# Performance work log

Measured on AMD Instinct MI355X. Metric: run time of the kernel, lower is better.

The kernel has to match this reference:

```python
import jax, jax.numpy as jnp
import numpy as np

T_Q, N_M, D = 2000, 100000, 1024

def setup_inputs() -> dict:
    key = jax.random.key(0)
    k1, k2, k3 = jax.random.split(key, 3)
    return {
        "query_seq": jax.random.normal(k1, (T_Q, D), dtype=jnp.float32),
        "matching_set": jax.random.normal(k2, (N_M, D), dtype=jnp.float32),
        "synth_set": jax.random.normal(k3, (N_M, D), dtype=jnp.float32),
        "topk": 4,
    }

def reference(query_seq, matching_set, synth_set, topk):
    # kNN-VC match: cosine distance, top-k nearest, mean of synth vectors.
    eps = jnp.asarray(1e-12, query_seq.dtype)
    q = query_seq / jnp.maximum(jnp.linalg.norm(query_seq, axis=-1, keepdims=True), eps)
    m = matching_set / jnp.maximum(jnp.linalg.norm(matching_set, axis=-1, keepdims=True), eps)
    dists = 1.0 - jnp.einsum("qd,nd->qn", q, m)  # (T_q, N_m) cosine distance
    _, idx = jax.lax.top_k(-dists, topk)          # k smallest distances
    # gather-average over selected synth vectors -> (T_q, D)
    out = jnp.mean(synth_set[idx], axis=1)
    return out
```

## Files before the change

kernel.cpp:

```cpp
#include <hip/hip_runtime.h>
#include <math.h>

#define T_Q    2000
#define N_M    100000
#define D_DIM  1024
#define QTILES 16
#define NTILES 782
#define MPAD   (NTILES * 128)
#define BK     32
#define KSTEPS (D_DIM / BK)
#define KST3   32
#define LDH    40
#define SSW    72
#define NC     16
#define QPAD   2048
#define TK     4

typedef _Float16 f16x8 __attribute__((ext_vector_type(8)));
typedef _Float16 f16x4 __attribute__((ext_vector_type(4)));
typedef float    f32x4 __attribute__((ext_vector_type(4)));
typedef unsigned int u32;

struct __align__(8) Cand { float v; int i; };
static_assert(sizeof(Cand) == 8, "cand size");

__device__ __forceinline__ bool better(float av, int ai, float bv, int bi) {
    return (av > bv) || (av == bv && ai < bi);
}

__device__ __forceinline__ f32x4 zero4() {
    f32x4 z; z[0] = 0.f; z[1] = 0.f; z[2] = 0.f; z[3] = 0.f; return z;
}

__device__ __forceinline__ void gload16(const _Float16* g, _Float16* l) {
    const __attribute__((address_space(1))) u32* gp =
        (const __attribute__((address_space(1))) u32*)g;
    __attribute__((address_space(3))) u32* lp =
        (__attribute__((address_space(3))) u32*)l;
    __builtin_amdgcn_global_load_lds(gp, lp, 16, 0, 0);
}

__device__ __forceinline__ int swz_s(int row) {
    return (row & 3) ^ ((row >> 2) & 1);
}

__global__ __launch_bounds__(256)
void knn_qcvt(const float* __restrict__ Qm, _Float16* __restrict__ Qh)
{
    const size_t base = (size_t)blockIdx.x * 2048 + (size_t)threadIdx.x * 8;
    const int row = (int)(base >> 10);
    const int hr  = (int)(base & 1023);
    f16x8 h;
    if (row < T_Q) {
        f32x4 a = *(const f32x4*)(Qm + base);
        f32x4 b = *(const f32x4*)(Qm + base + 4);
#pragma unroll
        for (int j = 0; j < 4; ++j) { h[j] = (_Float16)a[j]; h[4 + j] = (_Float16)b[j]; }
    } else {
#pragma unroll
        for (int j = 0; j < 8; ++j) h[j] = (_Float16)0.f;
    }
    const int g = hr >> 3;
    const int p = (g & ~3) | ((g & 3) ^ swz_s(row));
    *(f16x8*)(Qh + ((size_t)row << 10) + p * 8) = h;
}

__global__ __launch_bounds__(256)
void knn_qcvt_plain(const float* __restrict__ Qm, _Float16* __restrict__ Qh)
{
    const size_t base = (size_t)blockIdx.x * 2048 + (size_t)threadIdx.x * 8;
    const int row = (int)(base >> 10);
    f16x8 h;
    if (row < T_Q) {
        f32x4 a = *(const f32x4*)(Qm + base);
        f32x4 b = *(const f32x4*)(Qm + base + 4);
#pragma unroll
        for (int j = 0; j < 4; ++j) { h[j] = (_Float16)a[j]; h[4 + j] = (_Float16)b[j]; }
    } else {
#pragma unroll
        for (int j = 0; j < 8; ++j) h[j] = (_Float16)0.f;
    }
    *(f16x8*)(Qh + base) = h;
}

__global__ __launch_bounds__(256)
void knn_mcvt(const float* __restrict__ Mm, _Float16* __restrict__ Mh)
{
    const int wid  = threadIdx.x >> 6;
    const int lane = threadIdx.x & 63;
    const int r    = blockIdx.x * 4 + wid;
    f16x8 h0, h1;
    if (r < N_M) {
        const f32x4* mp = (const f32x4*)(Mm + (size_t)r * D_DIM) + lane * 4;
        f32x4 v0 = mp[0], v1 = mp[1], v2 = mp[2], v3 = mp[3];
        float ss = 0.f;
#pragma unroll
        for (int u = 0; u < 4; ++u)
            ss += v0[u] * v0[u] + v1[u] * v1[u] + v2[u] * v2[u] + v3[u] * v3[u];
#pragma unroll
        for (int off = 1; off <= 32; off <<= 1) ss += __shfl_xor(ss, off, 64);
        const float inv = ss > 0.f ? rsqrtf(ss) : 0.f;
#pragma unroll
        for (int u = 0; u < 4; ++u) {
            h0[u]     = (_Float16)(v0[u] * inv);
            h0[4 + u] = (_Float16)(v1[u] * inv);
            h1[u]     = (_Float16)(v2[u] * inv);
            h1[4 + u] = (_Float16)(v3[u] * inv);
        }
    } else {
#pragma unroll
        for (int j = 0; j < 8; ++j) { h0[j] = (_Float16)0.f; h1[j] = (_Float16)0.f; }
    }
    const int s  = swz_s(r);
    const int g0 = 2 * lane;
    const int g1 = g0 + 1;
    const int p0 = (g0 & ~3) | ((g0 & 3) ^ s);
    const int p1 = (g1 & ~3) | ((g1 & 3) ^ s);
    _Float16* base = Mh + (size_t)r * D_DIM;
    *(f16x8*)(base + p0 * 8) = h0;
    *(f16x8*)(base + p1 * 8) = h1;
}

__global__ __launch_bounds__(256, 4)
void knn_gemm_select_h(const _Float16* __restrict__ Qh,
                       const _Float16* __restrict__ Mh,
                       Cand* __restrict__ cand, int tpbn, int nsuper)
{
    __shared__ _Float16 As[2][128][32];
    __shared__ _Float16 Bs[2][128][32];

    const int bid   = blockIdx.x;
    const int c8    = bid & 7;
    const int jj0   = bid >> 3;
    const int qtile = jj0 & 15;
    const int sup   = c8 + 8 * (jj0 >> 4);

    const int nt0 = sup * tpbn;
    int nt1 = nt0 + tpbn;
    if (nt1 > NTILES) nt1 = NTILES;

    const int tid  = threadIdx.x;
    const int lane = tid & 63;
    const int wid  = tid >> 6;
    const int wr   = wid >> 1;
    const int wc   = wid & 1;
    const int l15  = lane & 15;
    const int lg   = lane >> 4;

    const int owner = wr * 4 + lg;

    float rv[4][TK]; int ri[4][TK];
#pragma unroll
    for (int q = 0; q < 4; ++q)
#pragma unroll
        for (int k = 0; k < TK; ++k) { rv[q][k] = -INFINITY; ri[q][k] = 0; }

    if (nt0 >= nt1) {
#pragma unroll
        for (int q = 0; q < 4; ++q) {
            const int qg = qtile * 128 + wc * 64 + q * 16 + l15;
            Cand* dst = cand + (((size_t)qg * nsuper + sup) * 8 + owner) * TK;
#pragma unroll
            for (int k = 0; k < TK; ++k) { Cand c; c.v = rv[q][k]; c.i = ri[q][k]; dst[k] = c; }
        }
        return;
    }

    const int srow   = tid >> 2;
    const int schunk = tid & 3;

    const _Float16* Bb = Qh + ((size_t)(qtile * 128 + srow) << 10) + schunk * 8;

    const int cp = (lg ^ (l15 & 3) ^ ((l15 >> 2) & 1)) * 8;

#define ISSUE_STEP(Abase, koff, bi) do {                                   \
        _Float16* ad_ = &As[bi][0][0] + tid * 8;                           \
        _Float16* bd_ = &Bs[bi][0][0] + tid * 8;                           \
        gload16((Abase) + (koff),               ad_);                      \
        gload16((Abase) + (64 << 10) + (koff),  ad_ + 2048);               \
        gload16(Bb + (koff),                    bd_);                      \
        gload16(Bb + (64 << 10) + (koff),       bd_ + 2048);               \
    } while (0)

    const _Float16* Ab = Mh + ((size_t)(nt0 * 128 + srow) << 10) + schunk * 8;
    int buf = 0;

    ISSUE_STEP(Ab, 0, 0);
    __syncthreads();

#pragma unroll 1
    for (int ntile = nt0; ntile < nt1; ++ntile) {
        const _Float16* AbNext = Ab + ((size_t)128 << 10);

        f32x4 acc[4][4];
#pragma unroll
        for (int i = 0; i < 4; ++i)
#pragma unroll
            for (int j = 0; j < 4; ++j) acc[i][j] = zero4();

#pragma unroll 1
        for (int t = 0; t < KST3; ++t) {
            if (t + 1 < KST3)            ISSUE_STEP(Ab, (t + 1) * 32, buf ^ 1);
            else if (ntile + 1 < nt1)    ISSUE_STEP(AbNext, 0, buf ^ 1);

            f16x8 af[4], bf[4];
#pragma unroll
            for (int f = 0; f < 4; ++f) {
                af[f] = *(const f16x8*)&As[buf][wr * 64 + f * 16 + l15][cp];
                bf[f] = *(const f16x8*)&Bs[buf][wc * 64 + f * 16 + l15][cp];
            }
#pragma unroll
            for (int i = 0; i < 4; ++i)
#pragma unroll
                for (int j = 0; j < 4; ++j)
                    acc[i][j] = __builtin_amdgcn_mfma_f32_16x16x32_f16(
                        af[i], bf[j], acc[i][j], 0, 0, 0);

            __syncthreads();
            buf ^= 1;
        }
        Ab = AbNext;

        const int rowbase = ntile * 128 + wr * 64 + lg * 4;
#pragma unroll
        for (int q = 0; q < 4; ++q) {
            float mx = acc[0][q][0];
#pragma unroll
            for (int i = 0; i < 4; ++i)
#pragma unroll
                for (int r = 0; r < 4; ++r) mx = fmaxf(mx, acc[i][q][r]);
            if (mx >= rv[q][TK - 1]) {
#pragma unroll
                for (int i = 0; i < 4; ++i)
#pragma unroll
                    for (int r = 0; r < 4; ++r) {
                        const int ng = rowbase + i * 16 + r;
                        float cv = acc[i][q][r];
                        if (ng < N_M && better(cv, ng, rv[q][TK - 1], ri[q][TK - 1])) {
                            int ci = ng;
#pragma unroll
                            for (int k = 0; k < TK; ++k) {
                                bool b = better(cv, ci, rv[q][k], ri[q][k]);
                                float nv = b ? cv : rv[q][k]; int ni = b ? ci : ri[q][k];
                                float ov = b ? rv[q][k] : cv; int oi = b ? ri[q][k] : ci;
                                rv[q][k] = nv; ri[q][k] = ni; cv = ov; ci = oi;
                            }
                        }
                    }
            }
        }
    }
#undef ISSUE_STEP

#pragma unroll
    for (int q = 0; q < 4; ++q) {
        const int qg = qtile * 128 + wc * 64 + q * 16 + l15;
        Cand* dst = cand + (((size_t)qg * nsuper + sup) * 8 + owner) * TK;
#pragma unroll
        for (int k = 0; k < TK; ++k) {
            Cand c; c.v = rv[q][k]; c.i = ri[q][k];
            dst[k] = c;
        }
    }
}

__global__ __launch_bounds__(64)
void knn_top16(const Cand* __restrict__ cand, int* __restrict__ top_idx, int ncand)
{
    __shared__ float lv[64][NC];
    __shared__ int   li[64][NC];

    const int q = blockIdx.x;
    const int lane = threadIdx.x;
    const Cand* rowp = cand + (size_t)q * ncand;

    float tv[NC]; int ti[NC];
#pragma unroll
    for (int k = 0; k < NC; ++k) { tv[k] = -INFINITY; ti[k] = 0; }

#pragma unroll 1
    for (int e = lane; e < ncand; e += 64) {
        Cand c = rowp[e];
        if (better(c.v, c.i, tv[NC - 1], ti[NC - 1])) {
            float cv = c.v; int ci = c.i;
#pragma unroll
            for (int k = 0; k < NC; ++k) {
                bool b = better(cv, ci, tv[k], ti[k]);
                float nv = b ? cv : tv[k]; int ni = b ? ci : ti[k];
                float ov = b ? tv[k] : cv; int oi = b ? ti[k] : ci;
                tv[k] = nv; ti[k] = ni; cv = ov; ci = oi;
            }
        }
    }

#pragma unroll
    for (int k = 0; k < NC; ++k) { lv[lane][k] = tv[k]; li[lane][k] = ti[k]; }
    __syncthreads();

    if (lane == 0) {
#pragma unroll 1
        for (int l = 1; l < 64; ++l) {
#pragma unroll 1
            for (int k = 0; k < NC; ++k) {
                float v = lv[l][k]; int i = li[l][k];
                if (!better(v, i, tv[NC - 1], ti[NC - 1])) break;
                float cv = v; int ci = i;
#pragma unroll
                for (int kk = 0; kk < NC; ++kk) {
                    bool b = better(cv, ci, tv[kk], ti[kk]);
                    float nv = b ? cv : tv[kk]; int ni = b ? ci : ti[kk];
                    float ov = b ? tv[kk] : cv; int oi = b ? ti[kk] : ci;
                    tv[kk] = nv; ti[kk] = ni; cv = ov; ci = oi;
                }
            }
        }
#pragma unroll
        for (int k = 0; k < NC; ++k) top_idx[q * NC + k] = ti[k];
    }
}

__global__ __launch_bounds__(256)
void knn_rescore(const float* __restrict__ Qm, const float* __restrict__ Mm,
                 const float* __restrict__ Sm, const int* __restrict__ topk_p,
                 const int* __restrict__ top_idx, float* __restrict__ outp)
{
    const int q   = blockIdx.x;
    const int tid = threadIdx.x;
    const int wid = tid >> 6, lane = tid & 63;

    __shared__ double sval[NC];
    __shared__ int    sidx[NC];
    __shared__ int    chosen[NC];

    int k = *topk_p;
    if (k > NC) k = NC;
    if (k < 1)  k = 1;

    const float* qrow = Qm + (size_t)q * D_DIM;
#pragma unroll 1
    for (int ci = wid; ci < NC; ci += 4) {
        int idx = top_idx[q * NC + ci];
        if (idx < 0)    idx = 0;
        if (idx >= N_M) idx = N_M - 1;
        const f32x4* mp = (const f32x4*)(Mm + (size_t)idx * D_DIM) + lane * 4;
        const f32x4* qp = (const f32x4*)qrow + lane * 4;
        double dot = 0.0, ss = 0.0;
#pragma unroll
        for (int j = 0; j < 4; ++j) {
            f32x4 mv = mp[j], qv = qp[j];
#pragma unroll
            for (int u = 0; u < 4; ++u) {
                dot += (double)mv[u] * (double)qv[u];
                ss  += (double)mv[u] * (double)mv[u];
            }
        }
#pragma unroll
        for (int off = 1; off <= 32; off <<= 1) {
            dot += __shfl_xor(dot, off, 64);
            ss  += __shfl_xor(ss, off, 64);
        }
        if (lane == 0) { sval[ci] = ss > 0.0 ? dot / sqrt(ss) : -1e300; sidx[ci] = idx; }
    }
    __syncthreads();

    if (tid == 0) {
        unsigned used = 0;
        for (int j = 0; j < k; ++j) {
            int best = -1;
            for (int i = 0; i < NC; ++i) {
                if (used & (1u << i)) continue;
                if (best < 0 || sval[i] > sval[best] ||
                    (sval[i] == sval[best] && sidx[i] < sidx[best])) best = i;
            }
            used |= 1u << best;
            chosen[j] = sidx[best];
        }
    }
    __syncthreads();

    const int d0 = tid * 4;
    f32x4 a = zero4();
    for (int j = 0; j < k; ++j) {
        f32x4 s4 = *(const f32x4*)(Sm + (size_t)chosen[j] * D_DIM + d0);
        a = a + s4;
    }
    const float inv = 1.0f / (float)k;
    a = a * inv;
    *(f32x4*)(outp + (size_t)q * D_DIM + d0) = a;
}

__global__ __launch_bounds__(256)
void knn_norms(const float* __restrict__ Mm, float* __restrict__ invn)
{
    const int wid  = threadIdx.x >> 6;
    const int lane = threadIdx.x & 63;
    const int r    = blockIdx.x * 4 + wid;
    if (r >= N_M) return;
    const f32x4* mp = (const f32x4*)(Mm + (size_t)r * D_DIM) + lane * 4;
    float ss = 0.f;
#pragma unroll
    for (int j = 0; j < 4; ++j) {
        f32x4 v = mp[j];
#pragma unroll
        for (int u = 0; u < 4; ++u) ss += v[u] * v[u];
    }
#pragma unroll
    for (int off = 1; off <= 32; off <<= 1) ss += __shfl_xor(ss, off, 64);
    if (lane == 0) invn[r] = ss > 0.f ? rsqrtf(ss) : 0.f;
}

__global__ __launch_bounds__(256)
void knn_gemm_select(const _Float16* __restrict__ Qh, const float* __restrict__ Mm,
                     const float* __restrict__ invn, Cand* __restrict__ cand,
                     int tpbn, int nsuper)
{
    __shared__ _Float16 As[128][LDH];
    __shared__ _Float16 Bs[128][LDH];
    __shared__ _Float16 Ss[128][SSW];
    __shared__ float    sinv[128];

    const int qtile = blockIdx.x & (QTILES - 1);
    const int sup   = blockIdx.x >> 4;
    const int nt0   = sup * tpbn;
    int nt1 = nt0 + tpbn;
    if (nt1 > NTILES) nt1 = NTILES;

    const int tid = threadIdx.x;
    const int row = tid >> 1;
    const int kh  = tid & 1;

    const int qrow_g = qtile * 128 + row;
    const _Float16* bbase = Qh + (size_t)qrow_g * D_DIM + kh * 16;

    const int lane = tid & 63;
    const int wid  = tid >> 6;
    const int wr   = wid >> 1;
    const int wc   = wid & 1;
    const int l15  = lane & 15;
    const int lg   = lane >> 4;

    float rv[NC]; int ri[NC];
#pragma unroll
    for (int k = 0; k < NC; ++k) { rv[k] = -INFINITY; ri[k] = 0; }

#pragma unroll 1
    for (int ntile = nt0; ntile < nt1; ++ntile) {
        const int nrow_g = ntile * 128 + row;
        const bool a_ok  = nrow_g < N_M;
        const float* abase = Mm + (size_t)nrow_g * D_DIM + kh * 16;

        f32x4 acc[4][4];
#pragma unroll
        for (int i = 0; i < 4; ++i)
#pragma unroll
            for (int j = 0; j < 4; ++j) acc[i][j] = zero4();

        f32x4 ar[4];
        f16x8 brh[2];
#pragma unroll
        for (int i = 0; i < 4; ++i) ar[i] = a_ok ? ((const f32x4*)abase)[i] : zero4();
        brh[0] = *(const f16x8*)(bbase);
        brh[1] = *(const f16x8*)(bbase + 8);

#pragma unroll 1
        for (int t = 0; t < KSTEPS; ++t) {
            __syncthreads();

            f16x8 ha0, ha1;
#pragma unroll
            for (int i = 0; i < 2; ++i)
#pragma unroll
                for (int j = 0; j < 4; ++j) {
                    ha0[i * 4 + j] = (_Float16)ar[i][j];
                    ha1[i * 4 + j] = (_Float16)ar[i + 2][j];
                }
            *(f16x8*)&As[row][kh * 16]     = ha0;
            *(f16x8*)&As[row][kh * 16 + 8] = ha1;
            *(f16x8*)&Bs[row][kh * 16]     = brh[0];
            *(f16x8*)&Bs[row][kh * 16 + 8] = brh[1];

            __syncthreads();

            if (t + 1 < KSTEPS) {
                const float*    ap = abase + (t + 1) * BK;
                const _Float16* bp = bbase + (t + 1) * BK;
#pragma unroll
                for (int i = 0; i < 4; ++i) ar[i] = a_ok ? ((const f32x4*)ap)[i] : zero4();
                brh[0] = *(const f16x8*)(bp);
                brh[1] = *(const f16x8*)(bp + 8);
            }

            f16x8 af[4], bf[4];
#pragma unroll
            for (int f = 0; f < 4; ++f) {
                af[f] = *(const f16x8*)&As[wr * 64 + f * 16 + l15][lg * 8];
                bf[f] = *(const f16x8*)&Bs[wc * 64 + f * 16 + l15][lg * 8];
            }
#pragma unroll
            for (int i = 0; i < 4; ++i)
#pragma unroll
                for (int j = 0; j < 4; ++j)
                    acc[i][j] = __builtin_amdgcn_mfma_f32_16x16x32_f16(
                        af[i], bf[j], acc[i][j], 0, 0, 0);
        }

        if (tid < 128) {
            const int r = ntile * 128 + tid;
            sinv[tid] = (r < N_M) ? invn[r] : 0.f;
        }

#pragma unroll 1
        for (int h = 0; h < 2; ++h) {
            __syncthreads();
            if (wr == h) {
#pragma unroll
                for (int fr = 0; fr < 4; ++fr)
#pragma unroll
                    for (int fc = 0; fc < 4; ++fc) {
                        f16x4 v;
#pragma unroll
                        for (int r = 0; r < 4; ++r) v[r] = (_Float16)acc[fr][fc][r];
                        *(f16x4*)&Ss[wc * 64 + fc * 16 + l15][fr * 16 + lg * 4] = v;
                    }
            }
            __syncthreads();

            if (tid < 128) {
                const int base = ntile * 128 + h * 64;
                int nval = N_M - base;
                if (nval > 64) nval = 64;
#pragma unroll 1
                for (int c = 0; c < nval; c += 8) {
                    f16x8 sv = *(const f16x8*)&Ss[tid][c];
                    f32x4 sa = *(const f32x4*)&sinv[h * 64 + c];
                    f32x4 sb = *(const f32x4*)&sinv[h * 64 + c + 4];
                    const int lim = (nval - c >= 8) ? 8 : (nval - c);
                    float s[8];
#pragma unroll
                    for (int j = 0; j < 4; ++j) {
                        s[j]     = (float)sv[j] * sa[j];
                        s[4 + j] = (float)sv[4 + j] * sb[j];
                    }
                    if (lim < 8)
#pragma unroll
                        for (int j = 0; j < 8; ++j)
                            if (j >= lim) s[j] = -INFINITY;
                    float m01 = fmaxf(s[0], s[1]), m23 = fmaxf(s[2], s[3]);
                    float m45 = fmaxf(s[4], s[5]), m67 = fmaxf(s[6], s[7]);
                    float mx = fmaxf(fmaxf(m01, m23), fmaxf(m45, m67));
                    if (mx >= rv[NC - 1]) {
#pragma unroll 1
                        for (int j = 0; j < 8; ++j) {
                            if (j >= lim) break;
                            float cv = s[j]; int ci = base + c + j;
                            if (better(cv, ci, rv[NC - 1], ri[NC - 1])) {
#pragma unroll
                                for (int k = 0; k < NC; ++k) {
                                    bool b = better(cv, ci, rv[k], ri[k]);
                                    float nv = b ? cv : rv[k]; int ni = b ? ci : ri[k];
                                    float ov = b ? rv[k] : cv; int oi = b ? ri[k] : ci;
                                    rv[k] = nv; ri[k] = ni; cv = ov; ci = oi;
                                }
                            }
                        }
                    }
                }
            }
        }
    }

    if (tid < 128) {
        const int qg = qtile * 128 + tid;
        Cand* dst = cand + ((size_t)qg * nsuper + sup) * NC;
#pragma unroll
        for (int k = 0; k < NC; ++k) { Cand c; c.v = rv[k]; c.i = ri[k]; dst[k] = c; }
    }
}

#define FNC 8
__global__ __launch_bounds__(256)
void knn_all(const float* __restrict__ Qm, const float* __restrict__ Mm,
             const float* __restrict__ Sm, const int* __restrict__ topk_p,
             float* __restrict__ outp)
{
    __shared__ float  qs[D_DIM];
    __shared__ float  wv[4][FNC];
    __shared__ int    wi[4][FNC];
    __shared__ int    cand8[FNC];
    __shared__ double dval[FNC];
    __shared__ int    chosen[FNC];
    __shared__ int    sk;

    const int q    = blockIdx.x;
    const int tid  = threadIdx.x;
    const int wid  = tid >> 6;
    const int lane = tid & 63;

    for (int i = tid; i < D_DIM / 4; i += 256)
        ((f32x4*)qs)[i] = ((const f32x4*)(Qm + (size_t)q * D_DIM))[i];
    __syncthreads();

    float tv[FNC]; int ti[FNC];
#pragma unroll
    for (int k = 0; k < FNC; ++k) { tv[k] = -INFINITY; ti[k] = 0; }

    for (int r = wid; r < N_M; r += 4) {
        const f32x4* mp = (const f32x4*)(Mm + (size_t)r * D_DIM) + lane * 4;
        const f32x4* qp = (const f32x4*)qs + lane * 4;
        float dot = 0.f, ss = 0.f;
#pragma unroll
        for (int j = 0; j < 4; ++j) {
            f32x4 mv = mp[j], qv = qp[j];
#pragma unroll
            for (int u = 0; u < 4; ++u) { dot += mv[u] * qv[u]; ss += mv[u] * mv[u]; }
        }
#pragma unroll
        for (int off = 1; off <= 32; off <<= 1) {
            dot += __shfl_xor(dot, off, 64);
            ss  += __shfl_xor(ss,  off, 64);
        }
        float s = ss > 0.f ? dot * rsqrtf(ss) : -INFINITY;
        if (better(s, r, tv[FNC - 1], ti[FNC - 1])) {
            float cv = s; int ci = r;
#pragma unroll
            for (int k = 0; k < FNC; ++k) {
                bool b = better(cv, ci, tv[k], ti[k]);
                float nv = b ? cv : tv[k]; int ni = b ? ci : ti[k];
                float ov = b ? tv[k] : cv; int oi = b ? ti[k] : ci;
                tv[k] = nv; ti[k] = ni; cv = ov; ci = oi;
            }
        }
    }

    if (lane == 0)
#pragma unroll
        for (int k = 0; k < FNC; ++k) { wv[wid][k] = tv[k]; wi[wid][k] = ti[k]; }
    __syncthreads();

    if (tid == 0) {
        unsigned used = 0;
        for (int j = 0; j < FNC; ++j) {
            float bv = -INFINITY; int bi = 0; int bs = -1;
            for (int s = 0; s < 4 * FNC; ++s) {
                if (used & (1u << s)) continue;
                float v = wv[s >> 3][s & 7]; int i = wi[s >> 3][s & 7];
                if (bs < 0 || better(v, i, bv, bi)) { bv = v; bi = i; bs = s; }
            }
            used |= 1u << bs;
            cand8[j] = bi;
        }
        int kk = *topk_p;
        if (kk < 1) kk = 1;
        if (kk > FNC) kk = FNC;
        sk = kk;
    }
    __syncthreads();

    for (int ci = wid; ci < FNC; ci += 4) {
        int idx = cand8[ci];
        if (idx < 0)     idx = 0;
        if (idx >= N_M)  idx = N_M - 1;
        const f32x4* mp = (const f32x4*)(Mm + (size_t)idx * D_DIM) + lane * 4;
        const f32x4* qp = (const f32x4*)qs + lane * 4;
        double dot = 0.0, ss = 0.0;
#pragma unroll
        for (int j = 0; j < 4; ++j) {
            f32x4 mv = mp[j], qv = qp[j];
#pragma unroll
            for (int u = 0; u < 4; ++u) {
                dot += (double)mv[u] * (double)qv[u];
                ss  += (double)mv[u] * (double)mv[u];
            }
        }
#pragma unroll
        for (int off = 1; off <= 32; off <<= 1) {
            dot += __shfl_xor(dot, off, 64);
            ss  += __shfl_xor(ss, off, 64);
        }
        if (lane == 0) dval[ci] = ss > 0.0 ? dot / sqrt(ss) : -1e300;
    }
    __syncthreads();

    if (tid == 0) {
        int kk = sk;
        unsigned used = 0;
        for (int j = 0; j < kk; ++j) {
            int best = -1;
            for (int i = 0; i < FNC; ++i) {
                if (used & (1u << i)) continue;
                if (best < 0 || dval[i] > dval[best] ||
                    (dval[i] == dval[best] && cand8[i] < cand8[best])) best = i;
            }
            used |= 1u << best;
            chosen[j] = cand8[best];
        }
    }
    __syncthreads();

    const int kk = sk;
    const int d0 = tid * 4;
    f32x4 a = zero4();
    for (int j = 0; j < kk; ++j) {
        f32x4 s4 = *(const f32x4*)(Sm + (size_t)chosen[j] * D_DIM + d0);
        a = a + s4;
    }
    const float inv = 1.0f / (float)kk;
    a = a * inv;
    *(f32x4*)(outp + (size_t)q * D_DIM + d0) = a;
}

extern "C" void kernel_launch(void* const* d_in, const int* in_sizes, int n_in,
                              void* d_out, int out_size, void* d_ws, size_t ws_size,
                              hipStream_t stream)
{
    (void)in_sizes; (void)n_in; (void)out_size;

    const float* Qm   = (const float*)d_in[0];
    const float* Mm   = (const float*)d_in[1];
    const float* Sm   = (const float*)d_in[2];
    const int*   topk = (const int*)d_in[3];
    float*       outp = (float*)d_out;

    const size_t A511      = 511;
    const size_t mh_bytes  = (((size_t)MPAD * D_DIM * sizeof(_Float16)) + A511) & ~A511;
    const size_t qh_bytes  = (size_t)QPAD * D_DIM * sizeof(_Float16);
    const size_t inv_bytes = ((size_t)N_M * sizeof(float) + A511) & ~A511;
    const size_t ti_bytes  = (((size_t)T_Q * NC * sizeof(int)) + A511) & ~A511;
    const size_t per_sup_m = (size_t)QPAD * 8 * TK * sizeof(Cand);
    const size_t per_sup_s = (size_t)QPAD * NC * sizeof(Cand);

    if (d_ws != nullptr) {
        const int ns_opts[5] = { 64, 48, 32, 16, 8 };
        int ns = 0;
        for (int i = 0; i < 5; ++i) {
            size_t need = mh_bytes + qh_bytes + ti_bytes + (size_t)ns_opts[i] * per_sup_m;
            if (need <= ws_size) { ns = ns_opts[i]; break; }
        }
        if (ns >= 8) {
            const int tpbn = (NTILES + ns - 1) / ns;

            _Float16* Mh      = (_Float16*)d_ws;
            _Float16* Qh      = (_Float16*)((char*)d_ws + mh_bytes);
            int*      top_idx = (int*)((char*)d_ws + mh_bytes + qh_bytes);
            Cand*     cand    = (Cand*)((char*)d_ws + mh_bytes + qh_bytes + ti_bytes);

            hipLaunchKernelGGL(knn_qcvt, dim3(QPAD * D_DIM / 2048), dim3(256), 0, stream,
                               Qm, Qh);
            hipLaunchKernelGGL(knn_mcvt, dim3(MPAD / 4), dim3(256), 0, stream,
                               Mm, Mh);
            hipLaunchKernelGGL(knn_gemm_select_h, dim3(QTILES * ns), dim3(256), 0, stream,
                               Qh, Mh, cand, tpbn, ns);
            hipLaunchKernelGGL(knn_top16, dim3(T_Q), dim3(64), 0, stream,
                               cand, top_idx, ns * 8 * TK);
            hipLaunchKernelGGL(knn_rescore, dim3(T_Q), dim3(256), 0, stream,
                               Qm, Mm, Sm, topk, top_idx, outp);
            return;
        }

        long long avail = (long long)ws_size
                        - (long long)(inv_bytes + qh_bytes + ti_bytes);
        int ns2 = avail > 0 ? (int)(avail / (long long)per_sup_s) : 0;
        if (ns2 > 64) ns2 = 64;
        if (ns2 >= 1) {
            int tpbn = (NTILES + ns2 - 1) / ns2;
            ns2 = (NTILES + tpbn - 1) / tpbn;

            float*    invn    = (float*)d_ws;
            _Float16* Qh      = (_Float16*)((char*)d_ws + inv_bytes);
            int*      top_idx = (int*)((char*)d_ws + inv_bytes + qh_bytes);
            Cand*     cand    = (Cand*)((char*)d_ws + inv_bytes + qh_bytes + ti_bytes);

            hipLaunchKernelGGL(knn_qcvt_plain, dim3(QPAD * D_DIM / 2048), dim3(256), 0, stream,
                               Qm, Qh);
            hipLaunchKernelGGL(knn_norms, dim3((N_M + 3) / 4), dim3(256), 0, stream,
                               Mm, invn);
            hipLaunchKernelGGL(knn_gemm_select, dim3(QTILES * ns2), dim3(256), 0, stream,
                               Qh, Mm, invn, cand, tpbn, ns2);
            hipLaunchKernelGGL(knn_top16, dim3(T_Q), dim3(64), 0, stream,
                               cand, top_idx, ns2 * NC);
            hipLaunchKernelGGL(knn_rescore, dim3(T_Q), dim3(256), 0, stream,
                               Qm, Mm, Sm, topk, top_idx, outp);
            return;
        }
    }

    hipLaunchKernelGGL(knn_all, dim3(T_Q), dim3(256), 0, stream,
                       Qm, Mm, Sm, topk, outp);
}
```

Baseline: 887.0 us.

## Pre-tile fp16 Q and M into contiguous per-k-step slabs with row-pair swizzle

The conversion kernels now write the normalized fp16 query and matching matrices in a blocked layout: each 128-row tile is stored as 32 contiguous 4096-element slabs, one per k-step, with rows paired and chunks XOR-swizzled. The GEMM's async global-to-LDS loads then read fully contiguous 8KB slabs instead of strided 64-byte row segments, and the LDS fragment offsets are recomputed to match the new swizzle. The aim is better global load coalescing and fewer LDS bank conflicts, in exchange for more complex index math and a layout coupling between the producer kernels and the GEMM.

```diff
diff --git a/kernel.cpp b/kernel.cpp
--- a/kernel.cpp
+++ b/kernel.cpp
@@ -10,6 +10,7 @@
 #define BK     32
 #define KSTEPS (D_DIM / BK)
 #define KST3   32
+#define SLABH  4096
 #define LDH    40
 #define SSW    72
 #define NC     16
@@ -40,16 +41,13 @@
     __builtin_amdgcn_global_load_lds(gp, lp, 16, 0, 0);
 }
 
-__device__ __forceinline__ int swz_s(int row) {
-    return (row & 3) ^ ((row >> 2) & 1);
-}
 
 __global__ __launch_bounds__(256)
 void knn_qcvt(const float* __restrict__ Qm, _Float16* __restrict__ Qh)
 {
     const size_t base = (size_t)blockIdx.x * 2048 + (size_t)threadIdx.x * 8;
     const int row = (int)(base >> 10);
-    const int hr  = (int)(base & 1023);
+    const int g   = (int)((base & 1023) >> 3);
     f16x8 h;
     if (row < T_Q) {
         f32x4 a = *(const f32x4*)(Qm + base);
@@ -60,9 +58,10 @@
 #pragma unroll
         for (int j = 0; j < 8; ++j) h[j] = (_Float16)0.f;
     }
-    const int g = hr >> 3;
-    const int p = (g & ~3) | ((g & 3) ^ swz_s(row));
-    *(f16x8*)(Qh + ((size_t)row << 10) + p * 8) = h;
+    const int nt = row >> 7, rt = row & 127, rr = rt >> 1, par = rt & 1;
+    const int t  = g >> 2,   d  = g & 3;
+    const int p  = rr * 8 + par * 4 + (d ^ (rr & 3));
+    *(f16x8*)(Qh + (((size_t)nt * 32 + t) * 512 + p) * 8) = h;
 }
 
 __global__ __launch_bounds__(256)
@@ -111,14 +110,15 @@
 #pragma unroll
         for (int j = 0; j < 8; ++j) { h0[j] = (_Float16)0.f; h1[j] = (_Float16)0.f; }
     }
-    const int s  = swz_s(r);
-    const int g0 = 2 * lane;
-    const int g1 = g0 + 1;
-    const int p0 = (g0 & ~3) | ((g0 & 3) ^ s);
-    const int p1 = (g1 & ~3) | ((g1 & 3) ^ s);
-    _Float16* base = Mh + (size_t)r * D_DIM;
-    *(f16x8*)(base + p0 * 8) = h0;
-    *(f16x8*)(base + p1 * 8) = h1;
+    const int nt = r >> 7, rt = r & 127, rr = rt >> 1, par = rt & 1;
+    const int s2 = rr & 3;
+    const int g0 = 2 * lane, g1 = g0 + 1;
+    const int t  = g0 >> 2;
+    const int p0 = rr * 8 + par * 4 + ((g0 & 3) ^ s2);
+    const int p1 = rr * 8 + par * 4 + ((g1 & 3) ^ s2);
+    _Float16* dst = Mh + ((size_t)nt * 32 + t) * 512 * 8;
+    *(f16x8*)(dst + (size_t)p0 * 8) = h0;
+    *(f16x8*)(dst + (size_t)p1 * 8) = h1;
 }
 
 __global__ __launch_bounds__(256, 4)
@@ -126,8 +126,8 @@
                        const _Float16* __restrict__ Mh,
                        Cand* __restrict__ cand, int tpbn, int nsuper)
 {
-    __shared__ _Float16 As[2][128][32];
-    __shared__ _Float16 Bs[2][128][32];
+    __shared__ _Float16 As[2][4096];
+    __shared__ _Float16 Bs[2][4096];
 
     const int bid   = blockIdx.x;
     const int c8    = bid & 7;
@@ -166,31 +166,32 @@
         return;
     }
 
-    const int srow   = tid >> 2;
-    const int schunk = tid & 3;
-
-    const _Float16* Bb = Qh + ((size_t)(qtile * 128 + srow) << 10) + schunk * 8;
-
-    const int cp = (lg ^ (l15 & 3) ^ ((l15 >> 2) & 1)) * 8;
-
-#define ISSUE_STEP(Abase, koff, bi) do {                                   \
-        _Float16* ad_ = &As[bi][0][0] + tid * 8;                           \
-        _Float16* bd_ = &Bs[bi][0][0] + tid * 8;                           \
-        gload16((Abase) + (koff),               ad_);                      \
-        gload16((Abase) + (64 << 10) + (koff),  ad_ + 2048);               \
-        gload16(Bb + (koff),                    bd_);                      \
-        gload16(Bb + (64 << 10) + (koff),       bd_ + 2048);               \
+    const int ch   = (l15 & 1) * 4 + (lg ^ ((l15 >> 1) & 3));
+    const int aoff = ((wr * 64 + l15) >> 1) * 64 + ch * 8;
+    const int boff = ((wc * 64 + l15) >> 1) * 64 + ch * 8;
+
+    const _Float16* Qt = Qh + (size_t)qtile * 32 * SLABH;
+
+#define ISSUE_STEP(TileA, tt, bi) do {                                     \
+        const _Float16* as_ = (TileA) + (size_t)(tt) * SLABH + tid * 8;    \
+        const _Float16* bs_ = Qt + (size_t)(tt) * SLABH + tid * 8;         \
+        _Float16* ad_ = &As[bi][0] + tid * 8;                              \
+        _Float16* bd_ = &Bs[bi][0] + tid * 8;                              \
+        gload16(as_,        ad_);                                          \
+        gload16(as_ + 2048, ad_ + 2048);                                   \
+        gload16(bs_,        bd_);                                          \
+        gload16(bs_ + 2048, bd_ + 2048);                                   \
     } while (0)
 
-    const _Float16* Ab = Mh + ((size_t)(nt0 * 128 + srow) << 10) + schunk * 8;
+    const _Float16* At = Mh + (size_t)nt0 * 32 * SLABH;
     int buf = 0;
 
-    ISSUE_STEP(Ab, 0, 0);
+    ISSUE_STEP(At, 0, 0);
     __syncthreads();
 
 #pragma unroll 1
     for (int ntile = nt0; ntile < nt1; ++ntile) {
-        const _Float16* AbNext = Ab + ((size_t)128 << 10);
+        const _Float16* AtNext = At + (size_t)32 * SLABH;
 
         f32x4 acc[4][4];
 #pragma unroll
@@ -200,14 +201,14 @@
 
 #pragma unroll 1
         for (int t = 0; t < KST3; ++t) {
-            if (t + 1 < KST3)            ISSUE_STEP(Ab, (t + 1) * 32, buf ^ 1);
-            else if (ntile + 1 < nt1)    ISSUE_STEP(AbNext, 0, buf ^ 1);
+            if (t + 1 < KST3)            ISSUE_STEP(At, t + 1, buf ^ 1);
+            else if (ntile + 1 < nt1)    ISSUE_STEP(AtNext, 0, buf ^ 1);
 
             f16x8 af[4], bf[4];
 #pragma unroll
             for (int f = 0; f < 4; ++f) {
-                af[f] = *(const f16x8*)&As[buf][wr * 64 + f * 16 + l15][cp];
-                bf[f] = *(const f16x8*)&Bs[buf][wc * 64 + f * 16 + l15][cp];
+                af[f] = *(const f16x8*)&As[buf][aoff + f * 512];
+                bf[f] = *(const f16x8*)&Bs[buf][boff + f * 512];
             }
 #pragma unroll
             for (int i = 0; i < 4; ++i)
@@ -219,7 +220,7 @@
             __syncthreads();
             buf ^= 1;
         }
-        Ab = AbNext;
+        At = AtNext;
 
         const int rowbase = ntile * 128 + wr * 64 + lg * 4;
 #pragma unroll
```

After: 1.067 ms. 1.2x slower.
